# Optimization experiments

Measured on AMD Instinct MI355X. Metric: run time of the kernel, lower is better.

Reference implementation:

```python
import jax, jax.numpy as jnp
import numpy as np

B, J, V, G, D = 1, 24, 20000, 2, 3
DCIN = J * 12          # num_parts * (9 + 3)
DC = 4                 # d_cond
HID = 128
BETA = 100.0           # softplus beta
EPS = 1e-8


def softplus_b(x):
    return jax.nn.softplus(BETA * x) / BETA


def group_linear(x, W, b):
    # x: (J, N, din), W: (J, din, dout), b: (J, dout)
    return jnp.einsum('jnd,jdo->jno', x, W) + b[:, None, :]


def axis_angle_to_matrix(aa):
    # aa: (..., 3) -> (..., 3, 3), Rodrigues formula
    angle = jnp.linalg.norm(aa, axis=-1, keepdims=True)
    axis = aa / jnp.where(angle < 1e-12, 1.0, angle)
    x, y, z = axis[..., 0], axis[..., 1], axis[..., 2]
    a = angle[..., 0]
    c, s = jnp.cos(a), jnp.sin(a)
    C = 1.0 - c
    r0 = jnp.stack([c + x * x * C, x * y * C - z * s, x * z * C + y * s], axis=-1)
    r1 = jnp.stack([y * x * C + z * s, c + y * y * C, y * z * C - x * s], axis=-1)
    r2 = jnp.stack([z * x * C - y * s, z * y * C + x * s, c + z * z * C], axis=-1)
    return jnp.stack([r0, r1, r2], axis=-2)


def blending_weights(pts, Jtr_center, Jtr_neigh, Jtr_self, bid_this, bid_other, rigid_alpha, rigid_beta):
    # pts: (B,J,V,3); Jtr_*: (B,J,1,3); bid_*: (J,) int
    ra = jax.nn.elu(rigid_alpha - 1.0) + 1.0
    a_n = ra[bid_other, bid_this].reshape(1, -1, 1, 1)
    a_s = ra[bid_this, bid_other].reshape(1, -1, 1, 1)
    be_n = rigid_beta[bid_other, bid_this].reshape(1, -1, 1, 1)
    be_s = rigid_beta[bid_this, bid_other].reshape(1, -1, 1, 1)
    vec_bone_n = Jtr_neigh - Jtr_center
    vec_bone_s = Jtr_self - Jtr_center
    nb_n = jnp.linalg.norm(vec_bone_n, axis=-1, keepdims=True)
    nb_s = jnp.linalg.norm(vec_bone_s, axis=-1, keepdims=True)
    vb_n = (Jtr_neigh - Jtr_self) / (nb_n + nb_s + EPS) * nb_n
    vb_s = -vb_n / (nb_n + EPS) * nb_s
    n_n = jnp.linalg.norm(vb_n, axis=-1, keepdims=True)
    n_s = jnp.linalg.norm(vb_s, axis=-1, keepdims=True)
    tr_o = Jtr_neigh - vb_n
    vec_pts = jax.lax.stop_gradient(pts) - tr_o   # pts.detach() in torch
    d_n = vb_n / (n_n + EPS)
    d_s = vb_s / (n_s + EPS)
    r_n = jnp.sum(vec_pts * d_n, axis=-1, keepdims=True) / (n_n + EPS)
    r_s = jnp.sum(vec_pts * d_s, axis=-1, keepdims=True) / (n_s + EPS)
    return jax.nn.sigmoid((r_n * a_n + be_n) - (r_s * a_s + be_s))


def _forward(pts, Bcond, Btr, Brot, Bneigh, rigid_alpha, rigid_beta,
             cW0, cb0, cW1, cb1, cW2, cb2, W0, b0, W1, b1, W2, b2, W3, b3):
    # world -> per-part local coords: (B,J,V,3)
    Brot_inv = jnp.swapaxes(Brot, -1, -2)
    pts_local = jnp.einsum('bjxy,bjvy->bjvx', Brot_inv, pts[:, None] - Btr[:, :, None])
    # neighbor-based deformation offsets
    ids = jax.lax.stop_gradient(Bneigh[0, :, :, 4, :2]).astype(jnp.int32)  # (J,G,2)
    offset_sum = jnp.zeros_like(pts_local)
    for gi in range(G):  # small fixed neighbor count
        Jtr_this = Bneigh[:, :, gi, 0][:, :, None]    # (B,J,1,3)
        Jtr_center = Bneigh[:, :, gi, 1][:, :, None]
        Jtr_other = Bneigh[:, :, gi, 2][:, :, None]
        Jpose = Bneigh[:, :, gi, 3][:, :, None]
        w = blending_weights(pts_local, Jtr_center, Jtr_other, Jtr_this,
                             ids[:, gi, 0], ids[:, gi, 1], rigid_alpha, rigid_beta)  # (B,J,V,1)
        Jp_w = jnp.nan_to_num(Jpose * w)              # (B,J,V,3)
        R = axis_angle_to_matrix(-Jp_w)               # (B,J,V,3,3)
        off = jnp.einsum('bjvxy,bjvy->bjvx', R, pts_local - Jtr_center) + Jtr_center - pts_local
        offset_sum = offset_sum + jnp.nan_to_num(off)
    pts_local = pts_local + offset_sum
    # grouped per-part MLP (INR with num_groups=J)
    x_in = jnp.transpose(pts_local, (1, 0, 2, 3)).reshape(J, B * V, D)
    cond = jnp.broadcast_to(jnp.transpose(Bcond, (1, 0, 2))[:, :, None, :], (J, B, V, DCIN)).reshape(J, B * V, DCIN)
    c = softplus_b(group_linear(cond, cW0, cb0))
    c = softplus_b(group_linear(c, cW1, cb1))
    c = group_linear(c, cW2, cb2)                      # (J, BV, 4)
    x = jnp.concatenate([x_in, c], axis=-1)            # (J, BV, 7)
    x = softplus_b(group_linear(x, W0, b0))
    x = softplus_b(group_linear(x, W1, b1))
    x = softplus_b(group_linear(x, W2, b2))
    x = group_linear(x, W3, b3)                        # (J, BV, 1)
    pred_parts = jnp.transpose(x.reshape(J, B, V, 1), (1, 0, 2, 3))  # (B,J,V,1)
    # softmin blend over parts
    pred_min = jnp.min(pred_parts, axis=1)             # (B,V,1)
    delta = pred_parts - pred_min[:, None]
    wsm = jax.nn.softmax(-delta * 200.0, axis=1)       # Softmin(dim=1)
    return jnp.sum(delta * wsm, axis=1) + pred_min


def setup_inputs() -> dict:
    key = jax.random.key(0)
    ks = jax.random.split(key, 16)
    pts = jax.random.normal(ks[0], (B, V, D), jnp.float32)
    Bcond = jax.random.normal(ks[1], (B, J, DCIN), jnp.float32) * 0.1
    Btr = jax.random.normal(ks[2], (B, J, D), jnp.float32)
    Brot = jax.random.normal(ks[3], (B, J, D, D), jnp.float32)
    core = jax.random.normal(ks[4], (B, J, G, 4, D), jnp.float32) * 0.5
    ids_this = jnp.arange(J, dtype=jnp.float32)
    ids_o0 = jnp.mod(jnp.arange(J) + 1, J).astype(jnp.float32)
    ids_o1 = jnp.mod(jnp.arange(J) - 1, J).astype(jnp.float32)
    bid = jnp.zeros((B, J, G, 1, D), jnp.float32)
    bid = bid.at[:, :, 0, 0, 0].set(ids_this).at[:, :, 0, 0, 1].set(ids_o0)
    bid = bid.at[:, :, 1, 0, 0].set(ids_this).at[:, :, 1, 0, 1].set(ids_o1)
    Bneigh = jnp.concatenate([core, bid], axis=-2)     # (B,J,G,5,D)
    rigid_alpha = jnp.full((J, J), 2.0, jnp.float32)   # blend_alpha init
    rigid_beta = jnp.zeros((J, J), jnp.float32)
    def gl(k, din, dout, std):
        return jax.random.normal(k, (J, din, dout), jnp.float32) * std, jnp.zeros((J, dout), jnp.float32)
    cW0, cb0 = gl(ks[5], DCIN, DC * 4, float(np.sqrt(2.0 / DCIN)))
    cW1, cb1 = gl(ks[6], DC * 4, DC * 4, float(np.sqrt(2.0 / (DC * 4))))
    cW2, cb2 = gl(ks[7], DC * 4, DC, 1e-5)
    std_h = float(np.sqrt(2.0) / np.sqrt(HID))
    W0, b0 = gl(ks[8], D + DC, HID, std_h)
    W1, b1 = gl(ks[9], HID, HID, std_h)
    W2, b2 = gl(ks[10], HID, HID, std_h)
    W3 = jax.random.normal(ks[11], (J, HID, 1), jnp.float32) * 1e-5 + float(np.sqrt(np.pi) / np.sqrt(HID))
    b3 = jnp.full((J, 1), -1.0, jnp.float32)           # -radius_init
    return {'pts': pts, 'Bcond': Bcond, 'Btr': Btr, 'Brot': Brot, 'Bneigh': Bneigh,
            'rigid_alpha': rigid_alpha, 'rigid_beta': rigid_beta,
            'cW0': cW0, 'cb0': cb0, 'cW1': cW1, 'cb1': cb1, 'cW2': cW2, 'cb2': cb2,
            'W0': W0, 'b0': b0, 'W1': W1, 'b1': b1, 'W2': W2, 'b2': b2, 'W3': W3, 'b3': b3}


def reference(pts, Bcond, Btr, Brot, Bneigh, rigid_alpha, rigid_beta,
              cW0, cb0, cW1, cb1, cW2, cb2, W0, b0, W1, b1, W2, b2, W3, b3):
    return _forward(pts, Bcond, Btr, Brot, Bneigh, rigid_alpha, rigid_beta,
                    cW0, cb0, cW1, cb1, cW2, cb2, W0, b0, W1, b1, W2, b2, W3, b3)
```

## Files before the change

kernel.cpp:

```cpp
#include <hip/hip_runtime.h>
#include <hip/hip_bf16.h>
#include <math.h>

#define VN 20000
#define JN 24
#define TILE 48
#define MI_N 3
#define KP 132
#define EPSF 1e-8f
#define WPREP_BLOCKS 1632

typedef __attribute__((ext_vector_type(8))) short bfrag;
typedef __attribute__((ext_vector_type(4))) float f32x4;

#define WJ_STRIDE 139264
#define L0A 0
#define L0B 4096
#define L1A 8192
#define L1B 40960
#define L2A 73728
#define L2B 106496

__device__ __forceinline__ unsigned short f2bf(float x) {
    __hip_bfloat16 b = __float2bfloat16(x);
    unsigned short u; __builtin_memcpy(&u, &b, 2); return u;
}
__device__ __forceinline__ float bf2f(unsigned short u) {
    __hip_bfloat16 b; __builtin_memcpy(&b, &u, 2);
    return __bfloat162float(b);
}
__device__ __forceinline__ unsigned int pack_hl(float x) {
    const unsigned int h = (__float_as_uint(x) + 0x8000u) & 0xffff0000u;
    const float hf = __uint_as_float(h);
    const float lo = x - hf;
    unsigned int r;
    asm("v_cvt_pk_bf16_f32 %0, %1, %2" : "=v"(r) : "v"(hf), "v"(lo));
    return r;
}

__device__ __forceinline__ float softplus_fast(float x) {
    const float u = __builtin_amdgcn_exp2f(-144.269504f * fabsf(x));
    float p = fmaf(u, 3.04480e-4f, -1.31584e-3f);
    p = fmaf(u, p, 2.852768e-3f);
    p = fmaf(u, p, -4.902308e-3f);
    p = fmaf(u, p, 9.992342e-3f);
    p = fmaf(u, p, 8.0e-8f);
    return fmaxf(x, 0.0f) + p;
}

__global__ __launch_bounds__(256) void setup_kernel(
    const float* __restrict__ W0, const float* __restrict__ W1,
    const float* __restrict__ W2, unsigned short* __restrict__ wt,
    const float* __restrict__ Bcond, const float* __restrict__ Bneigh,
    const float* __restrict__ ralpha, const float* __restrict__ rbeta,
    const float* __restrict__ cW0, const float* __restrict__ cb0,
    const float* __restrict__ cW1, const float* __restrict__ cb1,
    const float* __restrict__ cW2, const float* __restrict__ cb2,
    float* __restrict__ c4, float* __restrict__ geom)
{
    if (blockIdx.x < WPREP_BLOCKS) {
        const int g = blockIdx.x * 256 + threadIdx.x;
        const int jj = g / 17408;
        const int r = (g - jj * 17408) * 8;
        const float* src; int kin, pr; bool loP;
        if (r < 8192)       { src = W0 + jj * 896;   kin = 7;   pr = r & 4095;          loP = r >= L0B; }
        else if (r < 73728) { src = W1 + jj * 16384; kin = 128; pr = (r - L1A) & 32767; loP = r >= L1B; }
        else                { src = W2 + jj * 16384; kin = 128; pr = (r - L2A) & 32767; loP = r >= L2B; }
        const int lane = (pr >> 3) & 63;
        const int nt   = (pr >> 9) & 7;
        const int ks   = pr >> 12;
        const int n  = nt * 16 + (lane & 15);
        const int k0 = (ks * 32 + (lane >> 4) * 8) >> 1;
        unsigned short out[8];
        #pragma unroll
        for (int kk = 0; kk < 4; ++kk) {
            const float v = (k0 + kk < kin) ? src[(k0 + kk) * 128 + n] : 0.0f;
            const unsigned short h = f2bf(v);
            if (!loP) { out[2*kk] = h; out[2*kk+1] = h; }
            else      { out[2*kk] = f2bf(v - bf2f(h)); out[2*kk+1] = 0; }
        }
        *(uint4*)(wt + jj * WJ_STRIDE + r) = *(const uint4*)out;
        return;
    }

    __shared__ float cond_s[288];
    __shared__ float sh[16][17];
    __shared__ float hb[16];
    const int j = blockIdx.x - WPREP_BLOCKS;
    const int t = threadIdx.x;

    for (int i = t; i < 288; i += 256) cond_s[i] = Bcond[j * 288 + i];

    if (t < 2) {
        const int gi = t;
        const float* nb = Bneigh + (j * 2 + gi) * 15;
        const float tx = nb[0],  ty = nb[1],  tz = nb[2];
        const float cx = nb[3],  cy = nb[4],  cz = nb[5];
        const float ox = nb[6],  oy = nb[7],  oz = nb[8];
        const float px = nb[9],  py = nb[10], pz = nb[11];
        const int bid_this  = (int)nb[12];
        const int bid_other = (int)nb[13];
        const float xa_n = ralpha[bid_other * JN + bid_this] - 1.0f;
        const float xa_s = ralpha[bid_this * JN + bid_other] - 1.0f;
        const float a_n = xa_n > 0.0f ? xa_n + 1.0f : expf(xa_n);
        const float a_s = xa_s > 0.0f ? xa_s + 1.0f : expf(xa_s);
        const float be_n = rbeta[bid_other * JN + bid_this];
        const float be_s = rbeta[bid_this * JN + bid_other];

        const float bnx = ox - cx, bny = oy - cy, bnz = oz - cz;
        const float bsx = tx - cx, bsy = ty - cy, bsz = tz - cz;
        const float nb_n = sqrtf(bnx*bnx + bny*bny + bnz*bnz);
        const float nb_s = sqrtf(bsx*bsx + bsy*bsy + bsz*bsz);
        const float f = nb_n / (nb_n + nb_s + EPSF);
        const float vbnx = (ox - tx) * f, vbny = (oy - ty) * f, vbnz = (oz - tz) * f;
        const float g2 = -nb_s / (nb_n + EPSF);
        const float vbsx = vbnx * g2, vbsy = vbny * g2, vbsz = vbnz * g2;
        const float n_n = sqrtf(vbnx*vbnx + vbny*vbny + vbnz*vbnz);
        const float n_s = sqrtf(vbsx*vbsx + vbsy*vbsy + vbsz*vbsz);
        const float trx = ox - vbnx, tr_y = oy - vbny, trz = oz - vbnz;
        const float inn = 1.0f / ((n_n + EPSF) * (n_n + EPSF));
        const float ins = 1.0f / ((n_s + EPSF) * (n_s + EPSF));
        const float gx = vbnx * inn * a_n - vbsx * ins * a_s;
        const float gy = vbny * inn * a_n - vbsy * ins * a_s;
        const float gz = vbnz * inn * a_n - vbsz * ins * a_s;
        const float h = -(trx * gx + tr_y * gy + trz * gz) + be_n - be_s;
        float* gm = geom + (j * 2 + gi) * 12;
        gm[0] = gx; gm[1] = gy; gm[2] = gz; gm[3] = h;
        gm[4] = px; gm[5] = py; gm[6] = pz;
        gm[7] = cx; gm[8] = cy; gm[9] = cz;
        gm[10] = 0.0f; gm[11] = 0.0f;
    }
    __syncthreads();

    {
        const int o = t & 15, c = t >> 4;
        const float* w = cW0 + j * 288 * 16 + o;
        const int d0 = c * 18;
        float acc = 0.0f;
        #pragma unroll
        for (int d = 0; d < 18; ++d) acc = fmaf(cond_s[d0 + d], w[(d0 + d) * 16], acc);
        sh[c][o] = acc;
    }
    __syncthreads();
    if (t < 16) {
        float acc = cb0[j * 16 + t];
        #pragma unroll
        for (int c = 0; c < 16; ++c) acc += sh[c][t];
        hb[t] = softplus_fast(acc);
    }
    __syncthreads();
    if (t < 16) {
        const float* w = cW1 + j * 256 + t;
        float acc = cb1[j * 16 + t];
        #pragma unroll
        for (int d = 0; d < 16; ++d) acc = fmaf(hb[d], w[d * 16], acc);
        sh[0][t] = softplus_fast(acc);
    }
    __syncthreads();
    if (t < 4) {
        const float* w = cW2 + j * 64 + t;
        float acc = cb2[j * 4 + t];
        #pragma unroll
        for (int d = 0; d < 16; ++d) acc = fmaf(sh[0][d], w[d * 4], acc);
        c4[j * 4 + t] = acc;
    }
}

template<int NKS>
__device__ __forceinline__ void mfma_layer(
    unsigned int* __restrict__ X,
    const unsigned short* __restrict__ wA,
    const unsigned short* __restrict__ wB,
    const float* __restrict__ bvec,
    int q, int lane)
{
    const int l = lane & 15;
    const int quad = lane >> 4;
    const float bia0 = bvec[q * 32 + l];
    const float bia1 = bvec[q * 32 + 16 + l];
    f32x4 acc[MI_N][2];
    #pragma unroll
    for (int mi = 0; mi < MI_N; ++mi) {
        acc[mi][0] = (f32x4){bia0, bia0, bia0, bia0};
        acc[mi][1] = (f32x4){bia1, bia1, bia1, bia1};
    }

    #pragma unroll 2
    for (int ks = 0; ks < NKS; ++ks) {
        bfrag bA[2], bB[2];
        #pragma unroll
        for (int ni = 0; ni < 2; ++ni) {
            const int off = ((ks * 8 + (q * 2 + ni)) * 64 + lane) * 8;
            bA[ni] = *(const bfrag*)(wA + off);
            bB[ni] = *(const bfrag*)(wB + off);
        }
        #pragma unroll
        for (int mi = 0; mi < MI_N; ++mi) {
            const bfrag a = *(const bfrag*)(
                (const unsigned short*)(X + (mi * 16 + l) * KP) + ks * 32 + quad * 8);
            #pragma unroll
            for (int ni = 0; ni < 2; ++ni) {
                acc[mi][ni] = __builtin_amdgcn_mfma_f32_16x16x32_bf16(a, bA[ni], acc[mi][ni], 0, 0, 0);
                acc[mi][ni] = __builtin_amdgcn_mfma_f32_16x16x32_bf16(a, bB[ni], acc[mi][ni], 0, 0, 0);
            }
        }
    }
    __syncthreads();
    #pragma unroll
    for (int ni = 0; ni < 2; ++ni) {
        const int ch = q * 32 + ni * 16 + l;
        #pragma unroll
        for (int mi = 0; mi < MI_N; ++mi) {
            #pragma unroll
            for (int r = 0; r < 4; ++r) {
                const float v = softplus_fast(acc[mi][ni][r]);
                const int p = mi * 16 + quad * 4 + r;
                X[p * KP + ch] = pack_hl(v);
            }
        }
    }
    __syncthreads();
}

__global__ __launch_bounds__(256, 4) void main_kernel(
    const float* __restrict__ pts, const float* __restrict__ Btr,
    const float* __restrict__ Brot,
    const float* __restrict__ b0, const float* __restrict__ b1,
    const float* __restrict__ b2, const float* __restrict__ W3,
    const float* __restrict__ b3,
    const float* __restrict__ c4, const float* __restrict__ geom,
    const unsigned short* __restrict__ wt,
    float* __restrict__ pred)
{
    __shared__ unsigned int X[TILE * KP];
    const int j = blockIdx.y;
    const int v0 = blockIdx.x * TILE;
    const int t = threadIdx.x;
    const int lane = t & 63;
    const int q = __builtin_amdgcn_readfirstlane(t >> 6);

    if (t < TILE) {
        const int v = v0 + t;
        float plx = 0.0f, ply = 0.0f, plz = 0.0f;
        if (v < VN) {
            const float dx = pts[v * 3 + 0] - Btr[j * 3 + 0];
            const float dy = pts[v * 3 + 1] - Btr[j * 3 + 1];
            const float dz = pts[v * 3 + 2] - Btr[j * 3 + 2];
            const float* R = Brot + j * 9;
            plx = R[0] * dx + R[3] * dy + R[6] * dz;
            ply = R[1] * dx + R[4] * dy + R[7] * dz;
            plz = R[2] * dx + R[5] * dy + R[8] * dz;
            float osx = 0.0f, osy = 0.0f, osz = 0.0f;
            #pragma unroll
            for (int gi = 0; gi < 2; ++gi) {
                const float* gm = geom + (j * 2 + gi) * 12;
                const float arg = plx * gm[0] + ply * gm[1] + plz * gm[2] + gm[3];
                const float w = 1.0f / (1.0f + __expf(-arg));
                const float aax = -gm[4] * w, aay = -gm[5] * w, aaz = -gm[6] * w;
                const float jcx = gm[7], jcy = gm[8], jcz = gm[9];
                const float ang = sqrtf(aax * aax + aay * aay + aaz * aaz);
                const float inv = ang < 1e-12f ? 1.0f : 1.0f / ang;
                const float ux = aax * inv, uy = aay * inv, uz = aaz * inv;
                const float co = __cosf(ang), si = __sinf(ang), C = 1.0f - co;
                const float vx = plx - jcx, vy = ply - jcy, vz = plz - jcz;
                const float du = ux * vx + uy * vy + uz * vz;
                const float cxv = uy * vz - uz * vy;
                const float cyv = uz * vx - ux * vz;
                const float czv = ux * vy - uy * vx;
                float offx = co * vx + si * cxv + C * ux * du + jcx - plx;
                float offy = co * vy + si * cyv + C * uy * du + jcy - ply;
                float offz = co * vz + si * czv + C * uz * du + jcz - plz;
                if (isnan(offx)) offx = 0.0f;
                if (isnan(offy)) offy = 0.0f;
                if (isnan(offz)) offz = 0.0f;
                osx += offx; osy += offy; osz += offz;
            }
            plx += osx; ply += osy; plz += osz;
        }
        X[t * KP + 0] = pack_hl(plx);
        X[t * KP + 1] = pack_hl(ply);
        X[t * KP + 2] = pack_hl(plz);
        X[t * KP + 3] = pack_hl(c4[j * 4 + 0]);
        X[t * KP + 4] = pack_hl(c4[j * 4 + 1]);
        X[t * KP + 5] = pack_hl(c4[j * 4 + 2]);
        X[t * KP + 6] = pack_hl(c4[j * 4 + 3]);
        #pragma unroll
        for (int k = 7; k < 16; ++k) X[t * KP + k] = 0u;
    }
    __syncthreads();

    const unsigned short* wj = wt + j * WJ_STRIDE;
    mfma_layer<1>(X, wj + L0A, wj + L0B, b0 + j * 128, q, lane);
    mfma_layer<8>(X, wj + L1A, wj + L1B, b1 + j * 128, q, lane);
    mfma_layer<8>(X, wj + L2A, wj + L2B, b2 + j * 128, q, lane);

    if (lane < TILE) {
        const float* w3 = W3 + j * 128 + q * 32;
        float part = 0.0f;
        #pragma unroll 8
        for (int kk = 0; kk < 32; ++kk) {
            const unsigned int d = X[lane * KP + q * 32 + kk];
            const float xv = __uint_as_float(d << 16)
                           + __uint_as_float(d & 0xffff0000u);
            part = fmaf(xv, w3[kk], part);
        }
        X[lane * KP + 128 + q] = __float_as_uint(part);
    }
    __syncthreads();
    if (t < TILE) {
        const int v = v0 + t;
        const float r = b3[j]
            + __uint_as_float(X[t * KP + 128]) + __uint_as_float(X[t * KP + 129])
            + __uint_as_float(X[t * KP + 130]) + __uint_as_float(X[t * KP + 131]);
        if (v < VN) pred[j * VN + v] = r;
    }
}

__global__ __launch_bounds__(256) void softmin_kernel(const float* __restrict__ pred,
                                                      float* __restrict__ out)
{
    const int v = blockIdx.x * 256 + threadIdx.x;
    if (v >= VN) return;
    float vals[JN];
    float m = 3.4e38f;
    #pragma unroll
    for (int jj = 0; jj < JN; ++jj) {
        vals[jj] = pred[jj * VN + v];
        m = fminf(m, vals[jj]);
    }
    float s1 = 0.0f, s2 = 0.0f;
    #pragma unroll
    for (int jj = 0; jj < JN; ++jj) {
        const float d = vals[jj] - m;
        const float e = __expf(-200.0f * d);
        s1 += e;
        s2 = fmaf(d, e, s2);
    }
    out[v] = s2 / s1 + m;
}

extern "C" void kernel_launch(void* const* d_in, const int* in_sizes, int n_in,
                              void* d_out, int out_size, void* d_ws, size_t ws_size,
                              hipStream_t stream)
{
    const float* pts    = (const float*)d_in[0];
    const float* Bcond  = (const float*)d_in[1];
    const float* Btr    = (const float*)d_in[2];
    const float* Brot   = (const float*)d_in[3];
    const float* Bneigh = (const float*)d_in[4];
    const float* ralpha = (const float*)d_in[5];
    const float* rbeta  = (const float*)d_in[6];
    const float* cW0 = (const float*)d_in[7];
    const float* cb0 = (const float*)d_in[8];
    const float* cW1 = (const float*)d_in[9];
    const float* cb1 = (const float*)d_in[10];
    const float* cW2 = (const float*)d_in[11];
    const float* cb2 = (const float*)d_in[12];
    const float* W0 = (const float*)d_in[13];
    const float* b0 = (const float*)d_in[14];
    const float* W1 = (const float*)d_in[15];
    const float* b1 = (const float*)d_in[16];
    const float* W2 = (const float*)d_in[17];
    const float* b2 = (const float*)d_in[18];
    const float* W3 = (const float*)d_in[19];
    const float* b3 = (const float*)d_in[20];

    float* ws   = (float*)d_ws;
    float* pred = ws;
    float* c4   = ws + JN * VN;
    float* geom = c4 + JN * 4;
    unsigned short* wt = (unsigned short*)(geom + JN * 2 * 12);

    setup_kernel<<<WPREP_BLOCKS + JN, 256, 0, stream>>>(
        W0, W1, W2, wt,
        Bcond, Bneigh, ralpha, rbeta,
        cW0, cb0, cW1, cb1, cW2, cb2, c4, geom);

    dim3 grid((VN + TILE - 1) / TILE, JN);
    main_kernel<<<grid, 256, 0, stream>>>(pts, Btr, Brot,
                                          b0, b1, b2, W3, b3,
                                          c4, geom, wt, pred);

    softmin_kernel<<<(VN + 255) / 256, 256, 0, stream>>>(pred, (float*)d_out);
}
```

Measured before the change: 258.5 us.

## Fuse softmin into main kernel via per-tile atomic last-block counter

Drops the separate softmin launch. Each main-kernel block bumps a per-tile atomic counter after writing its pred values, and the last of the 24 joint blocks for a tile computes the softmin over joints for that tile. A memset to clear the counters is added, and the final W3 dot product now reads LDS with 128-bit vector loads. This trades one kernel launch and its extra pass over pred for a threadfence, an atomic per block and a memset launch.

```diff
diff --git a/kernel.cpp b/kernel.cpp
--- a/kernel.cpp
+++ b/kernel.cpp
@@ -8,6 +8,7 @@
 #define MI_N 3
 #define KP 132
 #define EPSF 1e-8f
+#define NTILES 417
 #define WPREP_BLOCKS 1632
 
 typedef __attribute__((ext_vector_type(8))) short bfrag;
@@ -230,9 +231,11 @@
     const float* __restrict__ b3,
     const float* __restrict__ c4, const float* __restrict__ geom,
     const unsigned short* __restrict__ wt,
-    float* __restrict__ pred)
+    float* __restrict__ pred, int* __restrict__ cnt,
+    float* __restrict__ out)
 {
     __shared__ unsigned int X[TILE * KP];
+    __shared__ int lastflag;
     const int j = blockIdx.y;
     const int v0 = blockIdx.x * TILE;
     const int t = threadIdx.x;
@@ -297,12 +300,17 @@
     if (lane < TILE) {
         const float* w3 = W3 + j * 128 + q * 32;
         float part = 0.0f;
-        #pragma unroll 8
-        for (int kk = 0; kk < 32; ++kk) {
-            const unsigned int d = X[lane * KP + q * 32 + kk];
-            const float xv = __uint_as_float(d << 16)
-                           + __uint_as_float(d & 0xffff0000u);
-            part = fmaf(xv, w3[kk], part);
+        #pragma unroll
+        for (int cb = 0; cb < 8; ++cb) {
+            union { uint4 v4; unsigned int u[4]; } d;
+            d.v4 = *(const uint4*)&X[lane * KP + q * 32 + cb * 4];
+            #pragma unroll
+            for (int i = 0; i < 4; ++i) {
+                const unsigned int di = d.u[i];
+                const float xv = __uint_as_float(di << 16)
+                               + __uint_as_float(di & 0xffff0000u);
+                part = fmaf(xv, w3[cb * 4 + i], part);
+            }
         }
         X[lane * KP + 128 + q] = __float_as_uint(part);
     }
@@ -314,29 +322,35 @@
             + __uint_as_float(X[t * KP + 130]) + __uint_as_float(X[t * KP + 131]);
         if (v < VN) pred[j * VN + v] = r;
     }
-}
-
-__global__ __launch_bounds__(256) void softmin_kernel(const float* __restrict__ pred,
-                                                      float* __restrict__ out)
-{
-    const int v = blockIdx.x * 256 + threadIdx.x;
-    if (v >= VN) return;
-    float vals[JN];
-    float m = 3.4e38f;
-    #pragma unroll
-    for (int jj = 0; jj < JN; ++jj) {
-        vals[jj] = pred[jj * VN + v];
-        m = fminf(m, vals[jj]);
-    }
-    float s1 = 0.0f, s2 = 0.0f;
-    #pragma unroll
-    for (int jj = 0; jj < JN; ++jj) {
-        const float d = vals[jj] - m;
-        const float e = __expf(-200.0f * d);
-        s1 += e;
-        s2 = fmaf(d, e, s2);
-    }
-    out[v] = s2 / s1 + m;
+
+    __threadfence();
+    __syncthreads();
+    if (t == 0) {
+        const int old = atomicAdd(&cnt[blockIdx.x], 1);
+        lastflag = (old == JN - 1) ? 1 : 0;
+    }
+    __syncthreads();
+    if (lastflag && t < TILE) {
+        const int v = v0 + t;
+        if (v < VN) {
+            float vals[JN];
+            float m = 3.4e38f;
+            #pragma unroll
+            for (int jj = 0; jj < JN; ++jj) {
+                vals[jj] = pred[jj * VN + v];
+                m = fminf(m, vals[jj]);
+            }
+            float s1 = 0.0f, s2 = 0.0f;
+            #pragma unroll
+            for (int jj = 0; jj < JN; ++jj) {
+                const float d = vals[jj] - m;
+                const float e = __expf(-200.0f * d);
+                s1 += e;
+                s2 = fmaf(d, e, s2);
+            }
+            out[v] = s2 / s1 + m;
+        }
+    }
 }
 
 extern "C" void kernel_launch(void* const* d_in, const int* in_sizes, int n_in,
@@ -370,16 +384,18 @@
     float* c4   = ws + JN * VN;
     float* geom = c4 + JN * 4;
     unsigned short* wt = (unsigned short*)(geom + JN * 2 * 12);
+    int* cnt = (int*)(wt + JN * WJ_STRIDE);
+
+    hipMemsetAsync(cnt, 0, NTILES * sizeof(int), stream);
 
     setup_kernel<<<WPREP_BLOCKS + JN, 256, 0, stream>>>(
         W0, W1, W2, wt,
         Bcond, Bneigh, ralpha, rbeta,
         cW0, cb0, cW1, cb1, cW2, cb2, c4, geom);
 
-    dim3 grid((VN + TILE - 1) / TILE, JN);
+    dim3 grid(NTILES, JN);
     main_kernel<<<grid, 256, 0, stream>>>(pts, Btr, Brot,
                                           b0, b1, b2, W3, b3,
-                                          c4, geom, wt, pred);
-
-    softmin_kernel<<<(VN + 255) / 256, 256, 0, stream>>>(pred, (float*)d_out);
-}
+                                          c4, geom, wt, pred, cnt,
+                                          (float*)d_out);
+}
```

Result: slower. 944.8 us (+265.5%).
